# Kernel tuning notes

Hardware: AMD Instinct MI355X
Metric: run time of the kernel (lower is better)

## Reference

```python
import jax, jax.numpy as jnp
import numpy as np

D_MODEL = 768
N_HEAD = 12
HEAD_DIM = D_MODEL // N_HEAD
D_FF = 4 * D_MODEL
EPS = 1e-5


def setup_inputs() -> dict:
    key = jax.random.key(0)
    ks = jax.random.split(key, 12)
    B, S = 4, 1024
    s = 0.02
    return {
        "x": jax.random.normal(ks[0], (B, S, D_MODEL), jnp.float32),
        "ln1_g": jnp.ones((D_MODEL,), jnp.float32),
        "ln1_b": jnp.zeros((D_MODEL,), jnp.float32),
        "ln2_g": jnp.ones((D_MODEL,), jnp.float32),
        "ln2_b": jnp.zeros((D_MODEL,), jnp.float32),
        "w_attn": jax.random.normal(ks[1], (D_MODEL, 3 * D_MODEL), jnp.float32) * s,
        "b_attn": jnp.zeros((3 * D_MODEL,), jnp.float32),
        "w_proj": jax.random.normal(ks[2], (D_MODEL, D_MODEL), jnp.float32) * s,
        "b_proj": jnp.zeros((D_MODEL,), jnp.float32),
        "w_fc": jax.random.normal(ks[3], (D_MODEL, D_FF), jnp.float32) * s,
        "b_fc": jnp.zeros((D_FF,), jnp.float32),
        "w_mlp_proj": jax.random.normal(ks[4], (D_FF, D_MODEL), jnp.float32) * s,
        "b_mlp_proj": jnpp.zeros((D_MODEL,), jnp.float32) if False else jnp.zeros((D_MODEL,), jnp.float32),
    }


def layer_norm(x, g, b):
    mu = jnp.mean(x, axis=-1, keepdims=True)
    var = jnp.mean(jnp.square(x - mu), axis=-1, keepdims=True)
    return (x - mu) * jax.lax.rsqrt(var + EPS) * g + b


def attention(x, w_attn, b_attn, w_proj, b_proj):
    B, S, _ = x.shape
    qkv = x @ w_attn + b_attn                      # [B,S,3D]
    q, k, v = jnp.split(qkv, 3, axis=-1)
    def heads(t):
        return t.reshape(B, S, N_HEAD, HEAD_DIM).transpose(0, 2, 1, 3)  # [B,H,S,hd]
    q, k, v = heads(q), heads(k), heads(v)
    scale = HEAD_DIM ** (-0.5)
    att = jnp.einsum("bhqd,bhkd->bhqk", q, k) * scale
    # additive causal mask: strictly-upper triangle gets -1e9 (matches TF source)
    mask = 1.0 - jnp.tril(jnp.ones((S, S), att.dtype))
    att = att + mask * (-1e9)
    att = jax.nn.softmax(att, axis=-1)
    y = jnp.einsum("bhqk,bhkd->bhqd", att, v)
    y = y.transpose(0, 2, 1, 3).reshape(B, S, D_MODEL)
    return y @ w_proj + b_proj


def mlp(x, w_fc, b_fc, w_mlp_proj, b_mlp_proj):
    h = jax.nn.gelu(x @ w_fc + b_fc, approximate=True)
    return h @ w_mlp_proj + b_mlp_proj


def reference(x, ln1_g, ln1_b, ln2_g, ln2_b, w_attn, b_attn, w_proj, b_proj,
              w_fc, b_fc, w_mlp_proj, b_mlp_proj):
    x = x + attention(layer_norm(x, ln1_g, ln1_b), w_attn, b_attn, w_proj, b_proj)
    x = x + mlp(layer_norm(x, ln2_g, ln2_b), w_fc, b_fc, w_mlp_proj, b_mlp_proj)
    return x
```

## Files before the change

### kernel.cpp

```cpp
#include <hip/hip_runtime.h>

typedef unsigned short u16;
typedef short bf8_t __attribute__((ext_vector_type(8)));
typedef float f32x4 __attribute__((ext_vector_type(4)));

__device__ __forceinline__ u16 f2bf(float f) {
  unsigned u = __builtin_bit_cast(unsigned, f);
  unsigned r = (u + 0x7fffu + ((u >> 16) & 1u)) >> 16;
  return (u16)r;
}

__device__ __forceinline__ float b2f(u16 v) {
  unsigned u = ((unsigned)v) << 16;
  return __builtin_bit_cast(float, u);
}

__device__ __forceinline__ void gld16(const void* g, void* l) {
  __builtin_amdgcn_global_load_lds((const __attribute__((address_space(1))) unsigned int*)g,
                                   (__attribute__((address_space(3))) unsigned int*)l, 16, 0, 0);
}

#define MFMA(a, b, c) __builtin_amdgcn_mfma_f32_16x16x32_bf16((a), (b), (c), 0, 0, 0)

__global__ void wtrans_kernel(const float* __restrict__ W, u16* __restrict__ WT, int K, int N) {
  __shared__ float tile[32][33];
  const int n0 = blockIdx.x << 5, k0 = blockIdx.y << 5;
  const int tx = threadIdx.x, ty = threadIdx.y;
#pragma unroll
  for (int i = 0; i < 4; i++) {
    const int r = ty + (i << 3);
    tile[r][tx] = W[(size_t)(k0 + r) * N + n0 + tx];
  }
  __syncthreads();
#pragma unroll
  for (int i = 0; i < 4; i++) {
    const int r = ty + (i << 3);
    WT[(size_t)(n0 + r) * K + k0 + tx] = f2bf(tile[tx][r]);
  }
}

__global__ void ln_kernel(const float* __restrict__ x, const float* __restrict__ g,
                          const float* __restrict__ bb, u16* __restrict__ o) {
  const int row = blockIdx.x, t = threadIdx.x;
  const float* xr = x + (size_t)row * 768;
  float v[3];
#pragma unroll
  for (int i = 0; i < 3; i++) v[i] = xr[t + (i << 8)];
  float s = v[0] + v[1] + v[2];
#pragma unroll
  for (int off = 1; off < 64; off <<= 1) s += __shfl_xor(s, off, 64);
  __shared__ float red[4];
  const int w = t >> 6;
  if ((t & 63) == 0) red[w] = s;
  __syncthreads();
  const float mu = (red[0] + red[1] + red[2] + red[3]) * (1.f / 768.f);
  float q = 0.f;
#pragma unroll
  for (int i = 0; i < 3; i++) {
    v[i] -= mu;
    q += v[i] * v[i];
  }
#pragma unroll
  for (int off = 1; off < 64; off <<= 1) q += __shfl_xor(q, off, 64);
  __syncthreads();
  if ((t & 63) == 0) red[w] = q;
  __syncthreads();
  const float var = (red[0] + red[1] + red[2] + red[3]) * (1.f / 768.f);
  const float rs = rsqrtf(var + 1e-5f);
#pragma unroll
  for (int i = 0; i < 3; i++) {
    const int idx = t + (i << 8);
    o[(size_t)row * 768 + idx] = f2bf(v[i] * rs * g[idx] + bb[idx]);
  }
}

template <int EPI>
__global__ void gemm_kernel(const u16* __restrict__ A, const u16* __restrict__ BT,
                            const float* __restrict__ bias, const float* __restrict__ res,
                            void* __restrict__ outp, int M, int N, int K, int kLen) {
  __shared__ __align__(16) u16 As[2][128 * 32];
  __shared__ __align__(16) u16 Bs[2][128 * 32];
  const int m0 = blockIdx.y << 7, n0 = blockIdx.x << 7;
  const int kOff = blockIdx.z * kLen;
  const int tid = threadIdx.x, lane = tid & 63, w = tid >> 6;
  const int wr = w >> 1, wc = w & 1;
  const int l16 = lane & 15, kg = lane >> 4;
  f32x4 acc[4][4];
  const f32x4 fz = {0.f, 0.f, 0.f, 0.f};
#pragma unroll
  for (int i = 0; i < 4; i++)
#pragma unroll
    for (int j = 0; j < 4; j++) acc[i][j] = fz;

  const int c1 = (w << 6) + lane;
  const int r1 = c1 >> 2, ko1 = (c1 & 3) << 3;
  const int c2 = c1 + 256;
  const int r2 = c2 >> 2, ko2 = (c2 & 3) << 3;
  const int lb1 = (c1 - lane) * 8, lb2 = (c2 - lane) * 8;

  auto stage = [&](int buf, int kt) {
    const int k0 = kOff + (kt << 5);
    gld16(A + (size_t)(m0 + r1) * K + k0 + ko1, As[buf] + lb1);
    gld16(A + (size_t)(m0 + r2) * K + k0 + ko2, As[buf] + lb2);
    gld16(BT + (size_t)(n0 + r1) * K + k0 + ko1, Bs[buf] + lb1);
    gld16(BT + (size_t)(n0 + r2) * K + k0 + ko2, Bs[buf] + lb2);
  };

  const int nkt = kLen >> 5;
  stage(0, 0);
  for (int kt = 0; kt < nkt; kt++) {
    const int cur = kt & 1;
    __syncthreads();
    if (kt + 1 < nkt) stage(cur ^ 1, kt + 1);
    bf8_t af[4], bfr[4];
#pragma unroll
    for (int mf = 0; mf < 4; mf++)
      af[mf] = *(const bf8_t*)&As[cur][((wr << 6) + (mf << 4) + l16) * 32 + (kg << 3)];
#pragma unroll
    for (int nf = 0; nf < 4; nf++)
      bfr[nf] = *(const bf8_t*)&Bs[cur][((wc << 6) + (nf << 4) + l16) * 32 + (kg << 3)];
#pragma unroll
    for (int mf = 0; mf < 4; mf++)
#pragma unroll
      for (int nf = 0; nf < 4; nf++) acc[mf][nf] = MFMA(af[mf], bfr[nf], acc[mf][nf]);
  }
  float* pout = (float*)outp + (size_t)blockIdx.z * M * N;
#pragma unroll
  for (int mf = 0; mf < 4; mf++) {
#pragma unroll
    for (int nf = 0; nf < 4; nf++) {
      const int col = n0 + (wc << 6) + (nf << 4) + l16;
      const float bv = (EPI == 3) ? 0.f : bias[col];
#pragma unroll
      for (int j = 0; j < 4; j++) {
        const int row = m0 + (wr << 6) + (mf << 4) + (kg << 2) + j;
        float v = acc[mf][nf][j] + bv;
        if constexpr (EPI == 0) {
          ((u16*)outp)[(size_t)row * N + col] = f2bf(v);
        } else if constexpr (EPI == 1) {
          const float u = 0.7978845608f * (v + 0.044715f * v * v * v);
          const float e = __expf(2.f * u);
          const float th = 1.f - 2.f / (e + 1.f);
          ((u16*)outp)[(size_t)row * N + col] = f2bf(0.5f * v * (1.f + th));
        } else if constexpr (EPI == 2) {
          v += res[(size_t)row * N + col];
          ((float*)outp)[(size_t)row * N + col] = v;
        } else {
          pout[(size_t)row * N + col] = v;
        }
      }
    }
  }
}

__global__ void reduce_kernel(const float* __restrict__ parts, const float* __restrict__ bias,
                              const float* __restrict__ res, float* __restrict__ out, int ns) {
  const int row = blockIdx.x, col = threadIdx.x << 2;
  const size_t base = (size_t)row * 768 + col;
  f32x4 a = *(const f32x4*)(parts + base);
  for (int s = 1; s < ns; s++) a += *(const f32x4*)(parts + (size_t)s * 4096 * 768 + base);
  const f32x4 bv = *(const f32x4*)(bias + col);
  const f32x4 rv = *(const f32x4*)(res + base);
  *(f32x4*)(out + base) = a + bv + rv;
}

template <bool SPLIT>
__global__ __launch_bounds__(256, 3) void attn_kernel(const u16* __restrict__ qkv,
                                                      u16* __restrict__ part_o,
                                                      float* __restrict__ partML,
                                                      u16* __restrict__ y) {
  __shared__ __align__(16) u16 Ks[2][64 * 64];
  __shared__ __align__(16) u16 Vt[2][64 * 64];
  __shared__ __align__(16) u16 Ps[4][16 * 72];
  int qt, c, t0, t1;
  if constexpr (SPLIT) {
    const int cid = 39 - (int)blockIdx.x;
    int g = 0, base = 0;
    while (cid >= base + 4 * (g + 1)) {
      base += 4 * (g + 1);
      g++;
    }
    const int r = cid - base;
    qt = (g << 2) + r / (g + 1);
    c = r % (g + 1);
    t0 = c << 2;
    t1 = min(t0 + 4, qt + 1);
  } else {
    qt = (int)gridDim.x - 1 - (int)blockIdx.x;
    c = 0;
    t0 = 0;
    t1 = qt + 1;
  }
  const int bh = blockIdx.y;
  const int b = bh / 12, h = bh - b * 12;
  const size_t brow = (size_t)b << 10;
  const int q0 = qt << 6;
  const int tid = threadIdx.x, lane = tid & 63, w = tid >> 6;
  const int l16 = lane & 15, kg = lane >> 4;

  const int c1 = tid, c2 = tid + 256;
  const int row1 = c1 >> 3, cc1 = c1 & 7;
  const int row2 = c2 >> 3, cc2 = c2 & 7;
  const int sw1 = ((cc1 ^ (row1 & 7)) << 3);
  const int sw2 = ((cc2 ^ (row2 & 7)) << 3);
  const int sg1 = ((cc1 & 1) << 2) | (cc1 & 2) | ((cc1 >> 2) & 1);
  const int sg2 = ((cc2 & 1) << 2) | (cc2 & 2) | ((cc2 >> 2) & 1);
  const int vcol1 = row1 ^ (sg1 << 3), d01 = cc1 << 3;
  const int vcol2 = row2 ^ (sg2 << 3), d02 = cc2 << 3;

  const int cbK = 768 + (h << 6), cbV = 1536 + (h << 6);

  const u16* Qbase = qkv + (brow + q0 + (w << 4) + l16) * 2304 + (h << 6) + (kg << 3);
  const bf8_t qf0 = *(const bf8_t*)(Qbase);
  const bf8_t qf1 = *(const bf8_t*)(Qbase + 32);

  gld16(qkv + (brow + (t0 << 6) + row1) * 2304 + cbK + sw1, Ks[t0 & 1] + (size_t)(c1 - lane) * 8);
  gld16(qkv + (brow + (t0 << 6) + row2) * 2304 + cbK + sw2, Ks[t0 & 1] + (size_t)(c2 - lane) * 8);
  bf8_t v1 = *(const bf8_t*)(qkv + (brow + (t0 << 6) + row1) * 2304 + cbV + (cc1 << 3));
  bf8_t v2 = *(const bf8_t*)(qkv + (brow + (t0 << 6) + row2) * 2304 + cbV + (cc2 << 3));

  f32x4 oacc[4];
  const f32x4 fz = {0.f, 0.f, 0.f, 0.f};
#pragma unroll
  for (int dg = 0; dg < 4; dg++) oacc[dg] = fz;
  float mrun[4], lrun[4];
#pragma unroll
  for (int j = 0; j < 4; j++) {
    mrun[j] = -1e30f;
    lrun[j] = 0.f;
  }

  for (int kt = t0; kt < t1; kt++) {
    const int cur = kt & 1;
    u16* Vc = Vt[cur];
#pragma unroll
    for (int i = 0; i < 8; i++) Vc[(d01 + i) * 64 + vcol1] = (u16)v1[i];
#pragma unroll
    for (int i = 0; i < 8; i++) Vc[(d02 + i) * 64 + vcol2] = (u16)v2[i];
    __syncthreads();

    if (kt + 1 < t1) {
      const int nr = (kt + 1) << 6;
      gld16(qkv + (brow + nr + row1) * 2304 + cbK + sw1, Ks[cur ^ 1] + (size_t)(c1 - lane) * 8);
      gld16(qkv + (brow + nr + row2) * 2304 + cbK + sw2, Ks[cur ^ 1] + (size_t)(c2 - lane) * 8);
      v1 = *(const bf8_t*)(qkv + (brow + nr + row1) * 2304 + cbV + (cc1 << 3));
      v2 = *(const bf8_t*)(qkv + (brow + nr + row2) * 2304 + cbV + (cc2 << 3));
    }

    const u16* Kc = Ks[cur];
    float sv[4][4];
#pragma unroll
    for (int g = 0; g < 4; g++) {
      f32x4 z = fz;
      const int key = (g << 4) + l16;
#pragma unroll
      for (int hd = 0; hd < 2; hd++) {
        const int ch = (kg + (hd << 2)) ^ (key & 7);
        const bf8_t kf = *(const bf8_t*)&Kc[key * 64 + (ch << 3)];
        z = MFMA(qf0, kf, z);
        if (hd == 0) {
        }
      }
      {
        const int ch0 = kg ^ (key & 7);
        const int ch1 = (kg + 4) ^ (key & 7);
        f32x4 zz = fz;
        zz = MFMA(qf0, *(const bf8_t*)&Kc[key * 64 + (ch0 << 3)], zz);
        zz = MFMA(qf1, *(const bf8_t*)&Kc[key * 64 + (ch1 << 3)], zz);
        z = zz;
      }
      const int gkey = (kt << 6) + key;
#pragma unroll
      for (int j = 0; j < 4; j++) {
        const int grow = q0 + (w << 4) + (kg << 2) + j;
        sv[g][j] = (gkey <= grow) ? z[j] * 0.125f : -1e30f;
      }
    }
    float tm[4];
#pragma unroll
    for (int j = 0; j < 4; j++)
      tm[j] = fmaxf(fmaxf(sv[0][j], sv[1][j]), fmaxf(sv[2][j], sv[3][j]));
#pragma unroll
    for (int o = 1; o < 16; o <<= 1)
#pragma unroll
      for (int j = 0; j < 4; j++) tm[j] = fmaxf(tm[j], __shfl_xor(tm[j], o, 64));
    float corr[4], tsum[4];
#pragma unroll
    for (int j = 0; j < 4; j++) {
      const float mn = fmaxf(mrun[j], tm[j]);
      corr[j] = __expf(mrun[j] - mn);
      mrun[j] = mn;
      tsum[j] = 0.f;
    }
#pragma unroll
    for (int g = 0; g < 4; g++)
#pragma unroll
      for (int j = 0; j < 4; j++) {
        const float p = __expf(sv[g][j] - mrun[j]);
        sv[g][j] = p;
        tsum[j] += p;
      }
#pragma unroll
    for (int o = 1; o < 16; o <<= 1)
#pragma unroll
      for (int j = 0; j < 4; j++) tsum[j] += __shfl_xor(tsum[j], o, 64);
#pragma unroll
    for (int j = 0; j < 4; j++) lrun[j] = lrun[j] * corr[j] + tsum[j];
#pragma unroll
    for (int dg = 0; dg < 4; dg++)
#pragma unroll
      for (int j = 0; j < 4; j++) oacc[dg][j] *= corr[j];
#pragma unroll
    for (int g = 0; g < 4; g++)
#pragma unroll
      for (int j = 0; j < 4; j++)
        Ps[w][((kg << 2) + j) * 72 + (g << 4) + l16] = f2bf(sv[g][j]);
    const bf8_t pf0 = *(const bf8_t*)&Ps[w][l16 * 72 + (kg << 3)];
    const bf8_t pf1 = *(const bf8_t*)&Ps[w][l16 * 72 + (kg << 3) + 32];
#pragma unroll
    for (int dg = 0; dg < 4; dg++) {
      const int sgr = (((l16 >> 3) & 1) << 2) | ((dg & 1) << 1) | (dg >> 1);
      const int d = (dg << 4) + l16;
      oacc[dg] = MFMA(pf0, *(const bf8_t*)&Vc[d * 64 + ((kg ^ sgr) << 3)], oacc[dg]);
      oacc[dg] = MFMA(pf1, *(const bf8_t*)&Vc[d * 64 + (((4 + kg) ^ sgr) << 3)], oacc[dg]);
    }
  }

  float inv[4];
#pragma unroll
  for (int j = 0; j < 4; j++) inv[j] = 1.f / lrun[j];
  if constexpr (SPLIT) {
    const int slot = (((bh << 4) + qt) << 2) + c;
    u16* po = part_o + (size_t)slot * 4096;
#pragma unroll
    for (int dg = 0; dg < 4; dg++)
#pragma unroll
      for (int j = 0; j < 4; j++)
        po[((w << 4) + (kg << 2) + j) * 64 + (dg << 4) + l16] = f2bf(oacc[dg][j] * inv[j]);
    if (l16 == 0) {
#pragma unroll
      for (int j = 0; j < 4; j++) {
        const int rr = (w << 4) + (kg << 2) + j;
        partML[(size_t)slot * 128 + rr * 2] = mrun[j];
        partML[(size_t)slot * 128 + rr * 2 + 1] = lrun[j];
      }
    }
  } else {
#pragma unroll
    for (int dg = 0; dg < 4; dg++)
#pragma unroll
      for (int j = 0; j < 4; j++) {
        const size_t grow = brow + q0 + (w << 4) + (kg << 2) + j;
        y[grow * 768 + (h << 6) + (dg << 4) + l16] = f2bf(oacc[dg][j] * inv[j]);
      }
  }
}

__global__ void attn_combine(const u16* __restrict__ part_o, const float* __restrict__ partML,
                             u16* __restrict__ y) {
  const int qt = blockIdx.x, bh = blockIdx.y;
  const int nc = (qt >> 2) + 1;
  const int tid = threadIdx.x;
  const int r = tid >> 2, cg = tid & 3;
  const int b = bh / 12, h = bh - b * 12;
  const int slot0 = ((bh << 4) + qt) << 2;
  float mv0 = -1e30f, mv1 = -1e30f, mv2 = -1e30f, mv3 = -1e30f;
  float lv0 = 0.f, lv1 = 0.f, lv2 = 0.f, lv3 = 0.f;
  mv0 = partML[(size_t)(slot0 + 0) * 128 + r * 2];
  lv0 = partML[(size_t)(slot0 + 0) * 128 + r * 2 + 1];
  if (nc > 1) {
    mv1 = partML[(size_t)(slot0 + 1) * 128 + r * 2];
    lv1 = partML[(size_t)(slot0 + 1) * 128 + r * 2 + 1];
  }
  if (nc > 2) {
    mv2 = partML[(size_t)(slot0 + 2) * 128 + r * 2];
    lv2 = partML[(size_t)(slot0 + 2) * 128 + r * 2 + 1];
  }
  if (nc > 3) {
    mv3 = partML[(size_t)(slot0 + 3) * 128 + r * 2];
    lv3 = partML[(size_t)(slot0 + 3) * 128 + r * 2 + 1];
  }
  const float M = fmaxf(fmaxf(mv0, mv1), fmaxf(mv2, mv3));
  const float w0 = __expf(mv0 - M) * lv0;
  const float w1 = (nc > 1) ? __expf(mv1 - M) * lv1 : 0.f;
  const float w2 = (nc > 2) ? __expf(mv2 - M) * lv2 : 0.f;
  const float w3 = (nc > 3) ? __expf(mv3 - M) * lv3 : 0.f;
  const float invL = 1.f / (w0 + w1 + w2 + w3);
  float acc[16];
#pragma unroll
  for (int i = 0; i < 16; i++) acc[i] = 0.f;
#pragma unroll
  for (int cc = 0; cc < 4; cc++) {
    if (cc < nc) {
      const float wv = (cc == 0) ? w0 : (cc == 1) ? w1 : (cc == 2) ? w2 : w3;
      const bf8_t* op = (const bf8_t*)(part_o + (size_t)(slot0 + cc) * 4096 + r * 64 + (cg << 4));
      const bf8_t o0 = op[0], o1 = op[1];
#pragma unroll
      for (int i = 0; i < 8; i++) {
        acc[i] += wv * b2f((u16)o0[i]);
        acc[8 + i] += wv * b2f((u16)o1[i]);
      }
    }
  }
  u16* yp = y + ((size_t)(b << 10) + (qt << 6) + r) * 768 + (h << 6) + (cg << 4);
#pragma unroll
  for (int i = 0; i < 16; i++) yp[i] = f2bf(acc[i] * invL);
}

extern "C" void kernel_launch(void* const* d_in, const int* in_sizes, int n_in,
                              void* d_out, int out_size, void* d_ws, size_t ws_size,
                              hipStream_t stream) {
  const float* x = (const float*)d_in[0];
  const float* ln1_g = (const float*)d_in[1];
  const float* ln1_b = (const float*)d_in[2];
  const float* ln2_g = (const float*)d_in[3];
  const float* ln2_b = (const float*)d_in[4];
  const float* w_attn = (const float*)d_in[5];
  const float* b_attn = (const float*)d_in[6];
  const float* w_proj = (const float*)d_in[7];
  const float* b_proj = (const float*)d_in[8];
  const float* w_fc = (const float*)d_in[9];
  const float* b_fc = (const float*)d_in[10];
  const float* w_mlp = (const float*)d_in[11];
  const float* b_mlp = (const float*)d_in[12];
  float* out = (float*)d_out;

  char* ws = (char*)d_ws;
  u16* wqkvT = (u16*)(ws + 0);
  u16* wprojT = (u16*)(ws + 3538944);
  u16* wfcT = (u16*)(ws + 4718592);
  u16* wmlpT = (u16*)(ws + 9437184);
  u16* xn = (u16*)(ws + 14155776);
  u16* qkv = (u16*)(ws + 20447232);
  u16* hbuf = (u16*)(ws + 20447232);
  u16* yb = (u16*)(ws + 45613056);
  float* x1 = (float*)(ws + 51904512);
  float* parts = (float*)(ws + 64487424);
  u16* part_o = (u16*)(ws + 64487424);
  float* partML = (float*)(ws + 89653248);

  const size_t PSZ = (size_t)4096 * 768 * 4;
  const int nsMlp = (ws_size >= 64487424 + 4 * PSZ) ? 4 : (ws_size >= 64487424 + 2 * PSZ ? 2 : 1);
  const int nsProj = (ws_size >= 64487424 + 2 * PSZ) ? 2 : 1;
  const bool useSplit = ws_size >= 91226112;

  const dim3 wtb(32, 8);
  wtrans_kernel<<<dim3(2304 / 32, 768 / 32), wtb, 0, stream>>>(w_attn, wqkvT, 768, 2304);
  wtrans_kernel<<<dim3(768 / 32, 768 / 32), wtb, 0, stream>>>(w_proj, wprojT, 768, 768);
  wtrans_kernel<<<dim3(3072 / 32, 768 / 32), wtb, 0, stream>>>(w_fc, wfcT, 768, 3072);
  wtrans_kernel<<<dim3(768 / 32, 3072 / 32), wtb, 0, stream>>>(w_mlp, wmlpT, 3072, 768);

  ln_kernel<<<4096, 256, 0, stream>>>(x, ln1_g, ln1_b, xn);
  gemm_kernel<0><<<dim3(18, 32), 256, 0, stream>>>(xn, wqkvT, b_attn, nullptr, qkv,
                                                   4096, 2304, 768, 768);
  if (useSplit) {
    attn_kernel<true><<<dim3(40, 48), 256, 0, stream>>>(qkv, part_o, partML, yb);
    attn_combine<<<dim3(16, 48), 256, 0, stream>>>(part_o, partML, yb);
  } else {
    attn_kernel<false><<<dim3(16, 48), 256, 0, stream>>>(qkv, part_o, partML, yb);
  }

  if (nsProj == 2) {
    gemm_kernel<3><<<dim3(6, 32, 2), 256, 0, stream>>>(yb, wprojT, nullptr, nullptr, parts,
                                                       4096, 768, 768, 384);
    reduce_kernel<<<4096, 192, 0, stream>>>(parts, b_proj, x, x1, 2);
  } else {
    gemm_kernel<2><<<dim3(6, 32), 256, 0, stream>>>(yb, wprojT, b_proj, x, x1,
                                                    4096, 768, 768, 768);
  }

  ln_kernel<<<4096, 256, 0, stream>>>(x1, ln2_g, ln2_b, xn);
  gemm_kernel<1><<<dim3(24, 32), 256, 0, stream>>>(xn, wfcT, b_fc, nullptr, hbuf,
                                                   4096, 3072, 768, 768);

  if (nsMlp > 1) {
    gemm_kernel<3><<<dim3(6, 32, nsMlp), 256, 0, stream>>>(hbuf, wmlpT, nullptr, nullptr, parts,
                                                           4096, 768, 3072, 3072 / nsMlp);
    reduce_kernel<<<4096, 192, 0, stream>>>(parts, b_mlp, x1, out, nsMlp);
  } else {
    gemm_kernel<2><<<dim3(6, 32), 256, 0, stream>>>(hbuf, wmlpT, b_mlp, x1, out,
                                                    4096, 768, 3072, 3072);
  }
}
```

Before: 204.2 us.

## Triple-buffer GEMM loads with explicit vmcnt waits; drop dead attention MFMAs

```diff
diff --git a/kernel.cpp b/kernel.cpp
--- a/kernel.cpp
+++ b/kernel.cpp
@@ -78,8 +78,8 @@
 __global__ void gemm_kernel(const u16* __restrict__ A, const u16* __restrict__ BT,
                             const float* __restrict__ bias, const float* __restrict__ res,
                             void* __restrict__ outp, int M, int N, int K, int kLen) {
-  __shared__ __align__(16) u16 As[2][128 * 32];
-  __shared__ __align__(16) u16 Bs[2][128 * 32];
+  __shared__ __align__(16) u16 As[3][128 * 32];
+  __shared__ __align__(16) u16 Bs[3][128 * 32];
   const int m0 = blockIdx.y << 7, n0 = blockIdx.x << 7;
   const int kOff = blockIdx.z * kLen;
   const int tid = threadIdx.x, lane = tid & 63, w = tid >> 6;
@@ -98,20 +98,33 @@
   const int r2 = c2 >> 2, ko2 = (c2 & 3) << 3;
   const int lb1 = (c1 - lane) * 8, lb2 = (c2 - lane) * 8;
 
-  auto stage = [&](int buf, int kt) {
-    const int k0 = kOff + (kt << 5);
-    gld16(A + (size_t)(m0 + r1) * K + k0 + ko1, As[buf] + lb1);
-    gld16(A + (size_t)(m0 + r2) * K + k0 + ko2, As[buf] + lb2);
-    gld16(BT + (size_t)(n0 + r1) * K + k0 + ko1, Bs[buf] + lb1);
-    gld16(BT + (size_t)(n0 + r2) * K + k0 + ko2, Bs[buf] + lb2);
-  };
+  const u16* Arow1 = A + (size_t)(m0 + r1) * K + kOff + ko1;
+  const u16* Arow2 = A + (size_t)(m0 + r2) * K + kOff + ko2;
+  const u16* Brow1 = BT + (size_t)(n0 + r1) * K + kOff + ko1;
+  const u16* Brow2 = BT + (size_t)(n0 + r2) * K + kOff + ko2;
+
+#define GSTAGE(buf_, kt_)                    \
+  do {                                       \
+    const int k0_ = (kt_) << 5;              \
+    gld16(Arow1 + k0_, As[buf_] + lb1);      \
+    gld16(Arow2 + k0_, As[buf_] + lb2);      \
+    gld16(Brow1 + k0_, Bs[buf_] + lb1);      \
+    gld16(Brow2 + k0_, Bs[buf_] + lb2);      \
+  } while (0)
 
   const int nkt = kLen >> 5;
-  stage(0, 0);
+  GSTAGE(0, 0);
+  if (nkt > 1) GSTAGE(1, 1);
+  int cur = 0, pre = 2;
   for (int kt = 0; kt < nkt; kt++) {
-    const int cur = kt & 1;
-    __syncthreads();
-    if (kt + 1 < nkt) stage(cur ^ 1, kt + 1);
+    if (kt + 1 < nkt) {
+      asm volatile("s_waitcnt vmcnt(4)" ::: "memory");
+    } else {
+      asm volatile("s_waitcnt vmcnt(0)" ::: "memory");
+    }
+    __builtin_amdgcn_s_barrier();
+    __builtin_amdgcn_sched_barrier(0);
+    if (kt + 2 < nkt) GSTAGE(pre, kt + 2);
     bf8_t af[4], bfr[4];
 #pragma unroll
     for (int mf = 0; mf < 4; mf++)
@@ -123,7 +136,10 @@
     for (int mf = 0; mf < 4; mf++)
 #pragma unroll
       for (int nf = 0; nf < 4; nf++) acc[mf][nf] = MFMA(af[mf], bfr[nf], acc[mf][nf]);
-  }
+    cur = (cur == 2) ? 0 : cur + 1;
+    pre = (pre == 2) ? 0 : pre + 1;
+  }
+#undef GSTAGE
   float* pout = (float*)outp + (size_t)blockIdx.z * M * N;
 #pragma unroll
   for (int mf = 0; mf < 4; mf++) {
@@ -251,24 +267,12 @@
     float sv[4][4];
 #pragma unroll
     for (int g = 0; g < 4; g++) {
+      const int key = (g << 4) + l16;
+      const int ch0 = kg ^ (key & 7);
+      const int ch1 = (kg + 4) ^ (key & 7);
       f32x4 z = fz;
-      const int key = (g << 4) + l16;
-#pragma unroll
-      for (int hd = 0; hd < 2; hd++) {
-        const int ch = (kg + (hd << 2)) ^ (key & 7);
-        const bf8_t kf = *(const bf8_t*)&Kc[key * 64 + (ch << 3)];
-        z = MFMA(qf0, kf, z);
-        if (hd == 0) {
-        }
-      }
-      {
-        const int ch0 = kg ^ (key & 7);
-        const int ch1 = (kg + 4) ^ (key & 7);
-        f32x4 zz = fz;
-        zz = MFMA(qf0, *(const bf8_t*)&Kc[key * 64 + (ch0 << 3)], zz);
-        zz = MFMA(qf1, *(const bf8_t*)&Kc[key * 64 + (ch1 << 3)], zz);
-        z = zz;
-      }
+      z = MFMA(qf0, *(const bf8_t*)&Kc[key * 64 + (ch0 << 3)], z);
+      z = MFMA(qf1, *(const bf8_t*)&Kc[key * 64 + (ch1 << 3)], z);
       const int gkey = (kt << 6) + key;
 #pragma unroll
       for (int j = 0; j < 4; j++) {
```

Measured after the change: 204.5 us. About the same (+0.1%).
